# Kernel optimization log

Measured on AMD Instinct MI355X. Metric: run time of the kernel, lower is better.

The kernel has to match this reference:

```python
import jax, jax.numpy as jnp
import numpy as np

D_MODEL = 1024
NUM_HEADS = 16
D_K = D_MODEL // NUM_HEADS
B, S = 2, 2048


def setup_inputs() -> dict:
    key = jax.random.key(0)
    ks = jax.random.split(key, 9)
    scale = 1.0 / np.sqrt(D_MODEL)
    return {
        "hidden_states": jax.random.normal(ks[0], (B, S, D_MODEL), dtype=jnp.float32),
        "attention_mask": jnp.ones((B, S, S), dtype=jnp.int32),
        "Wq": jax.random.normal(ks[1], (D_MODEL, D_MODEL), dtype=jnp.float32) * scale,
        "bq": jnp.zeros((D_MODEL,), dtype=jnp.float32),
        "Wk": jax.random.normal(ks[2], (D_MODEL, D_MODEL), dtype=jnp.float32) * scale,
        "bk": jnp.zeros((D_MODEL,), dtype=jnp.float32),
        "Wv": jax.random.normal(ks[3], (D_MODEL, D_MODEL), dtype=jnp.float32) * scale,
        "bv": jnp.zeros((D_MODEL,), dtype=jnp.float32),
        "Wo": jax.random.normal(ks[4], (D_MODEL, D_MODEL), dtype=jnp.float32) * scale,
        "bo": jnp.zeros((D_MODEL,), dtype=jnp.float32),
    }


def reference(hidden_states, attention_mask, Wq, bq, Wk, bk, Wv, bv, Wo, bo):
    b, s, _ = hidden_states.shape
    # torch Linear: y = x @ W.T + b
    def proj(W, bias):
        y = jnp.einsum('bsd,ed->bse', hidden_states, W) + bias
        return y.reshape(b, s, NUM_HEADS, D_K).transpose(0, 2, 1, 3)  # [B,H,S,dk]
    q = proj(Wq, bq)
    k = proj(Wk, bk)
    v = proj(Wv, bv)
    scores = jnp.einsum('bnqd,bnkd->bnqk', q, k) / np.sqrt(D_K)
    mask = attention_mask[:, None, :, :]  # [B,1,S,S]
    scores = jnp.where(mask == 0, jnp.float32(-1e9), scores)
    attn = jax.nn.softmax(scores, axis=-1)  # dropout = identity (eval)
    ctx = jnp.einsum('bnqk,bnkd->bnqd', attn, v)
    ctx = ctx.transpose(0, 2, 1, 3).reshape(b, s, D_MODEL)
    return jnp.einsum('bsd,ed->bse', ctx, Wo) + bo
```

## Files before the change

### kernel.cpp

```cpp
#include <hip/hip_runtime.h>

typedef short short8 __attribute__((ext_vector_type(8)));
typedef float floatx4 __attribute__((ext_vector_type(4)));
typedef unsigned short ushort4v __attribute__((ext_vector_type(4)));

#define DEV static __device__ __forceinline__

DEV unsigned short f2bf(float f) {
  unsigned int u = __builtin_bit_cast(unsigned int, f);
  u += 0x7fffu + ((u >> 16) & 1u);
  return (unsigned short)(u >> 16);
}

DEV unsigned int pkbf2(float a, float b) {
  unsigned int ua = __builtin_bit_cast(unsigned int, a) + 0x8000u;
  unsigned int ub = __builtin_bit_cast(unsigned int, b) + 0x8000u;
  return (ua >> 16) | (ub & 0xffff0000u);
}

DEV void gload16(const unsigned short* g, unsigned short* l) {
  __builtin_amdgcn_global_load_lds((__attribute__((address_space(1))) void*)g,
                                   (__attribute__((address_space(3))) void*)l,
                                   16, 0, 0);
}

__global__ void convert_kernel(const float* __restrict__ hs, const float* __restrict__ Wq,
                               const float* __restrict__ Wk, const float* __restrict__ Wv,
                               const float* __restrict__ Wo,
                               unsigned short* __restrict__ xbf, unsigned short* __restrict__ wqkv,
                               unsigned short* __restrict__ wobf) {
  size_t i4 = ((size_t)blockIdx.x * 256 + threadIdx.x) * 4;
  const float* src;
  unsigned short* dst;
  if (i4 < 4194304) {
    src = hs + i4; dst = xbf + i4;
  } else if (i4 < 7340032) {
    size_t o = i4 - 4194304;
    size_t lo = o & 1048575;
    src = (o < 1048576) ? (Wq + lo) : ((o < 2097152) ? (Wk + lo) : (Wv + lo));
    dst = wqkv + o;
  } else {
    size_t o = i4 - 7340032;
    src = Wo + o; dst = wobf + o;
  }
  float4 v = *(const float4*)src;
  ushort4v u;
  u.x = f2bf(v.x); u.y = f2bf(v.y); u.z = f2bf(v.z); u.w = f2bf(v.w);
  *(ushort4v*)dst = u;
}

__global__ void maskpack_kernel(const int* __restrict__ mask, unsigned long long* __restrict__ bits) {
  int w = blockIdx.x * 256 + threadIdx.x;
  const int4* p = (const int4*)(mask + (size_t)w * 64);
  unsigned long long r = 0ull;
#pragma unroll
  for (int j = 0; j < 16; ++j) {
    int4 m = p[j];
    r |= (unsigned long long)(m.x != 0) << (j * 4 + 0);
    r |= (unsigned long long)(m.y != 0) << (j * 4 + 1);
    r |= (unsigned long long)(m.z != 0) << (j * 4 + 2);
    r |= (unsigned long long)(m.w != 0) << (j * 4 + 3);
  }
  bits[w] = r;
}

__global__ void __launch_bounds__(256) qkv_gemm(
    const unsigned short* __restrict__ X, const unsigned short* __restrict__ W,
    const float* __restrict__ bq, const float* __restrict__ bk, const float* __restrict__ bv,
    unsigned short* __restrict__ Qb, unsigned short* __restrict__ Kb,
    unsigned short* __restrict__ Vt) {
  __shared__ __align__(16) unsigned short As[128 * 32];
  __shared__ __align__(16) unsigned short Bs[128 * 32];
  const int tid = threadIdx.x;
  const int lane = tid & 63, wv = tid >> 6;
  const int wm = wv >> 1, wn = wv & 1;
  const int quad = lane >> 4, l15 = lane & 15;
  const int mb = blockIdx.y, nb = blockIdx.x;

  const unsigned short* ga = X + (size_t)(mb * 128 + (tid >> 2)) * 1024 + (tid & 3) * 8;
  const unsigned short* gb = W + (size_t)(nb * 128 + (tid >> 2)) * 1024 + (tid & 3) * 8;
  unsigned short* la1 = As + tid * 8;
  unsigned short* la2 = As + 2048 + tid * 8;
  unsigned short* lb1 = Bs + tid * 8;
  unsigned short* lb2 = Bs + 2048 + tid * 8;

  floatx4 acc[4][4] = {};
  for (int kt = 0; kt < 32; ++kt) {
    const int k0 = kt * 32;
    gload16(ga + k0, la1);
    gload16(ga + k0 + 65536, la2);
    gload16(gb + k0, lb1);
    gload16(gb + k0 + 65536, lb2);
    __syncthreads();
    short8 af[4], bfr[4];
#pragma unroll
    for (int i = 0; i < 4; ++i) {
      af[i]  = *(const short8*)&As[(wm * 64 + i * 16 + l15) * 32 + quad * 8];
      bfr[i] = *(const short8*)&Bs[(wn * 64 + i * 16 + l15) * 32 + quad * 8];
    }
#pragma unroll
    for (int mt = 0; mt < 4; ++mt)
#pragma unroll
      for (int nt = 0; nt < 4; ++nt)
        acc[mt][nt] = __builtin_amdgcn_mfma_f32_16x16x32_bf16(af[mt], bfr[nt], acc[mt][nt], 0, 0, 0);
    __syncthreads();
  }
#pragma unroll
  for (int nt = 0; nt < 4; ++nt) {
    const int col = nb * 128 + wn * 64 + nt * 16 + l15;
    const int mat = col >> 10, nl = col & 1023;
    const float bias = (mat == 0) ? bq[nl] : ((mat == 1) ? bk[nl] : bv[nl]);
    const int h = nl >> 6, d = nl & 63;
#pragma unroll
    for (int mt = 0; mt < 4; ++mt) {
      const int row0 = mb * 128 + wm * 64 + mt * 16 + quad * 4;
      const int b_ = row0 >> 11, s = row0 & 2047;
      if (mat == 2) {
        ushort4v pv;
#pragma unroll
        for (int r = 0; r < 4; ++r) pv[r] = f2bf(acc[mt][nt][r] + bias);
        *(ushort4v*)&Vt[((size_t)(b_ * 16 + h) * 64 + d) * 2048 + s] = pv;
      } else {
#pragma unroll
        for (int r = 0; r < 4; ++r) {
          const unsigned short v = f2bf(acc[mt][nt][r] + bias);
          if (mat == 0) Qb[((size_t)(b_ * 16 + h) * 2048 + s + r) * 64 + d] = v;
          else          Kb[((size_t)(b_ * 16 + h) * 2048 + s + r) * 64 + d] = v;
        }
      }
    }
  }
}

__global__ void __launch_bounds__(256, 4) attn_kernel(
    const unsigned short* __restrict__ Qb, const unsigned short* __restrict__ Kb,
    const unsigned short* __restrict__ Vt, const unsigned long long* __restrict__ mbits,
    unsigned short* __restrict__ ctx) {
  __shared__ __align__(16) unsigned short Ks[128 * 64];
  __shared__ __align__(16) unsigned short Vs[64 * 128];
  const int tid = threadIdx.x;
  const int lane = tid & 63, wv = tid >> 6;
  const int quad = lane >> 4, l15 = lane & 15;
  const int pair = blockIdx.x >> 5, qt = blockIdx.x & 31;
  const int b_ = pair >> 4, h = pair & 15;
  const int qg = qt * 64 + wv * 16 + l15;
  const size_t pbase = (size_t)pair * (2048 * 64);

  short8 qf[2];
#pragma unroll
  for (int ks = 0; ks < 2; ++ks)
    qf[ks] = *(const short8*)(Qb + pbase + (size_t)qg * 64 + ks * 32 + quad * 8);

  floatx4 acc_o[4] = {};
  float lsum = 0.f;
  const float SCL = 0.125f * 1.44269504088896340736f;
  const float NC = -10.0f;

  for (int kb = 0; kb < 16; ++kb) {
    __syncthreads();
#pragma unroll
    for (int it = 0; it < 4; ++it) {
      const int row = it * 32 + (tid >> 3);
      const int c = tid & 7;
      short8 v = *(const short8*)(Kb + pbase + (size_t)(kb * 128 + row) * 64 + c * 8);
      *(short8*)&Ks[row * 64 + ((c ^ (row & 7)) * 8)] = v;
    }
#pragma unroll
    for (int it = 0; it < 4; ++it) {
      const int row = it * 16 + (tid >> 4);
      const int c = tid & 15;
      short8 v = *(const short8*)(Vt + (size_t)pair * (64 * 2048) + (size_t)row * 2048 + kb * 128 + c * 8);
      *(short8*)&Vs[row * 128 + ((c ^ (row & 7)) * 8)] = v;
    }
    __syncthreads();

    const unsigned long long* mrow = mbits + ((size_t)b_ * 2048 + qg) * 32 + kb * 2;
    const unsigned long long w0 = mrow[0], w1 = mrow[1];

    floatx4 accs[8] = {};
#pragma unroll
    for (int ks = 0; ks < 2; ++ks)
#pragma unroll
      for (int mt = 0; mt < 8; ++mt) {
        const int krow = mt * 16 + l15;
        short8 kf = *(const short8*)&Ks[krow * 64 + (((ks * 4 + quad) ^ (krow & 7)) * 8)];
        accs[mt] = __builtin_amdgcn_mfma_f32_16x16x32_bf16(kf, qf[ks], accs[mt], 0, 0, 0);
      }

    if (__any((w0 & w1) != ~0ull)) {
      const unsigned long long wq0 = w0 >> (quad * 4);
      const unsigned long long wq1 = w1 >> (quad * 4);
#pragma unroll
      for (int ntb = 0; ntb < 8; ++ntb) {
        const unsigned long long w = (ntb < 4) ? wq0 : wq1;
#pragma unroll
        for (int r = 0; r < 4; ++r)
          if (!((w >> ((ntb & 3) * 16 + r)) & 1ull)) accs[ntb][r] = -6e9f;
      }
    }

    unsigned int pk[8][2];
#pragma unroll
    for (int ntb = 0; ntb < 8; ++ntb) {
      const float p0 = exp2f(fmaf(accs[ntb][0], SCL, NC));
      const float p1 = exp2f(fmaf(accs[ntb][1], SCL, NC));
      const float p2 = exp2f(fmaf(accs[ntb][2], SCL, NC));
      const float p3 = exp2f(fmaf(accs[ntb][3], SCL, NC));
      lsum += (p0 + p1) + (p2 + p3);
      pk[ntb][0] = pkbf2(p0, p1);
      pk[ntb][1] = pkbf2(p2, p3);
    }

#pragma unroll
    for (int ks = 0; ks < 4; ++ks) {
      const int srcA = (quad & 1) * 32 + l15;
      const int hi = quad >> 1;
      unsigned int u0a = __shfl(pk[2 * ks][0], srcA),      u0b = __shfl(pk[2 * ks + 1][0], srcA);
      unsigned int u1a = __shfl(pk[2 * ks][1], srcA),      u1b = __shfl(pk[2 * ks + 1][1], srcA);
      unsigned int u2a = __shfl(pk[2 * ks][0], srcA + 16), u2b = __shfl(pk[2 * ks + 1][0], srcA + 16);
      unsigned int u3a = __shfl(pk[2 * ks][1], srcA + 16), u3b = __shfl(pk[2 * ks + 1][1], srcA + 16);
      union { unsigned int u[4]; short8 s8; } af;
      af.u[0] = hi ? u0b : u0a;
      af.u[1] = hi ? u1b : u1a;
      af.u[2] = hi ? u2b : u2a;
      af.u[3] = hi ? u3b : u3a;
#pragma unroll
      for (int nt = 0; nt < 4; ++nt) {
        const int vrow = nt * 16 + l15;
        short8 vf = *(const short8*)&Vs[vrow * 128 + (((ks * 4 + quad) ^ (vrow & 7)) * 8)];
        acc_o[nt] = __builtin_amdgcn_mfma_f32_16x16x32_bf16(af.s8, vf, acc_o[nt], 0, 0, 0);
      }
    }
  }

  lsum += __shfl_xor(lsum, 16);
  lsum += __shfl_xor(lsum, 32);
  float rl[4];
#pragma unroll
  for (int r = 0; r < 4; ++r) {
    const float lr = __shfl(lsum, (lane & 48) | (quad * 4 + r));
    rl[r] = 1.f / ((lr > 0.f) ? lr : 1.f);
  }
#pragma unroll
  for (int nt = 0; nt < 4; ++nt)
#pragma unroll
    for (int r = 0; r < 4; ++r) {
      const int rowg = qt * 64 + wv * 16 + quad * 4 + r;
      ctx[((size_t)b_ * 2048 + rowg) * 1024 + h * 64 + nt * 16 + l15] =
          f2bf(acc_o[nt][r] * rl[r]);
    }
}

__global__ void __launch_bounds__(256) out_gemm(
    const unsigned short* __restrict__ C, const unsigned short* __restrict__ W,
    const float* __restrict__ bo, float* __restrict__ out) {
  __shared__ __align__(16) unsigned short As[128 * 32];
  __shared__ __align__(16) unsigned short Bs[128 * 32];
  const int tid = threadIdx.x;
  const int lane = tid & 63, wv = tid >> 6;
  const int wm = wv >> 1, wn = wv & 1;
  const int quad = lane >> 4, l15 = lane & 15;
  const int mb = blockIdx.y, nb = blockIdx.x;

  const unsigned short* ga = C + (size_t)(mb * 128 + (tid >> 2)) * 1024 + (tid & 3) * 8;
  const unsigned short* gb = W + (size_t)(nb * 128 + (tid >> 2)) * 1024 + (tid & 3) * 8;
  unsigned short* la1 = As + tid * 8;
  unsigned short* la2 = As + 2048 + tid * 8;
  unsigned short* lb1 = Bs + tid * 8;
  unsigned short* lb2 = Bs + 2048 + tid * 8;

  floatx4 acc[4][4] = {};
  for (int kt = 0; kt < 32; ++kt) {
    const int k0 = kt * 32;
    gload16(ga + k0, la1);
    gload16(ga + k0 + 65536, la2);
    gload16(gb + k0, lb1);
    gload16(gb + k0 + 65536, lb2);
    __syncthreads();
    short8 af[4], bfr[4];
#pragma unroll
    for (int i = 0; i < 4; ++i) {
      af[i]  = *(const short8*)&As[(wm * 64 + i * 16 + l15) * 32 + quad * 8];
      bfr[i] = *(const short8*)&Bs[(wn * 64 + i * 16 + l15) * 32 + quad * 8];
    }
#pragma unroll
    for (int mt = 0; mt < 4; ++mt)
#pragma unroll
      for (int nt = 0; nt < 4; ++nt)
        acc[mt][nt] = __builtin_amdgcn_mfma_f32_16x16x32_bf16(af[mt], bfr[nt], acc[mt][nt], 0, 0, 0);
    __syncthreads();
  }
#pragma unroll
  for (int nt = 0; nt < 4; ++nt) {
    const int col = nb * 128 + wn * 64 + nt * 16 + l15;
    const float bias = bo[col];
#pragma unroll
    for (int mt = 0; mt < 4; ++mt)
#pragma unroll
      for (int r = 0; r < 4; ++r) {
        const int row = mb * 128 + wm * 64 + mt * 16 + quad * 4 + r;
        out[(size_t)row * 1024 + col] = acc[mt][nt][r] + bias;
      }
  }
}

extern "C" void kernel_launch(void* const* d_in, const int* in_sizes, int n_in,
                              void* d_out, int out_size, void* d_ws, size_t ws_size,
                              hipStream_t stream) {
  const float* hs = (const float*)d_in[0];
  const int* mask = (const int*)d_in[1];
  const float* Wq = (const float*)d_in[2];
  const float* bq = (const float*)d_in[3];
  const float* Wk = (const float*)d_in[4];
  const float* bk = (const float*)d_in[5];
  const float* Wv = (const float*)d_in[6];
  const float* bv = (const float*)d_in[7];
  const float* Wo = (const float*)d_in[8];
  const float* bo = (const float*)d_in[9];
  float* out = (float*)d_out;

  char* ws = (char*)d_ws;
  unsigned short* xbf  = (unsigned short*)(ws + 0);
  unsigned short* wqkv = (unsigned short*)(ws + 8388608);
  unsigned short* wobf = (unsigned short*)(ws + 14680064);
  unsigned short* Qb   = (unsigned short*)(ws + 16777216);
  unsigned short* Kb   = (unsigned short*)(ws + 25165824);
  unsigned short* Vt   = (unsigned short*)(ws + 33554432);
  unsigned short* ctx  = (unsigned short*)(ws + 41943040);
  unsigned long long* mbits = (unsigned long long*)(ws + 50331648);

  convert_kernel<<<8192, 256, 0, stream>>>(hs, Wq, Wk, Wv, Wo, xbf, wqkv, wobf);
  maskpack_kernel<<<512, 256, 0, stream>>>(mask, mbits);
  qkv_gemm<<<dim3(24, 32), 256, 0, stream>>>(xbf, wqkv, bq, bk, bv, Qb, Kb, Vt);
  attn_kernel<<<1024, 256, 0, stream>>>(Qb, Kb, Vt, mbits, ctx);
  out_gemm<<<dim3(8, 32), 256, 0, stream>>>(ctx, wobf, bo, out);
}
```

Baseline: 269.6 us.

## Use 32x32 MFMA in attention with 2-wave blocks; vectorize Q/K stores in QKV GEMM

The attention kernel switches from 16x16x32 to 32x32x16 bf16 MFMA. Each of two waves now handles 32 query rows, and the P matrix is exchanged with a single xor-32 shuffle instead of many cross-lane shuffles. The V LDS swizzle is adjusted to match the new fragment layout. The QKV GEMM swaps operands for the Q/K column blocks so each lane writes four contiguous bf16 values as one vector store with float4 bias loads, instead of scattered 2-byte stores. The larger MFMA tiles raise register pressure, and smaller blocks change occupancy and per-block K/V load work.

```diff
diff --git a/kernel.cpp b/kernel.cpp
--- a/kernel.cpp
+++ b/kernel.cpp
@@ -2,6 +2,7 @@
 
 typedef short short8 __attribute__((ext_vector_type(8)));
 typedef float floatx4 __attribute__((ext_vector_type(4)));
+typedef float floatx16 __attribute__((ext_vector_type(16)));
 typedef unsigned short ushort4v __attribute__((ext_vector_type(4)));
 
 #define DEV static __device__ __forceinline__
@@ -76,6 +77,7 @@
   const int wm = wv >> 1, wn = wv & 1;
   const int quad = lane >> 4, l15 = lane & 15;
   const int mb = blockIdx.y, nb = blockIdx.x;
+  const bool sw = (nb < 16);
 
   const unsigned short* ga = X + (size_t)(mb * 128 + (tid >> 2)) * 1024 + (tid & 3) * 8;
   const unsigned short* gb = W + (size_t)(nb * 128 + (tid >> 2)) * 1024 + (tid & 3) * 8;
@@ -83,6 +85,9 @@
   unsigned short* la2 = As + 2048 + tid * 8;
   unsigned short* lb1 = Bs + tid * 8;
   unsigned short* lb2 = Bs + 2048 + tid * 8;
+
+  const int wx = sw ? wn : wm;
+  const int ww = sw ? wm : wn;
 
   floatx4 acc[4][4] = {};
   for (int kt = 0; kt < 32; ++kt) {
@@ -92,47 +97,70 @@
     gload16(gb + k0, lb1);
     gload16(gb + k0 + 65536, lb2);
     __syncthreads();
-    short8 af[4], bfr[4];
+    short8 xa[4], wb[4];
 #pragma unroll
     for (int i = 0; i < 4; ++i) {
-      af[i]  = *(const short8*)&As[(wm * 64 + i * 16 + l15) * 32 + quad * 8];
-      bfr[i] = *(const short8*)&Bs[(wn * 64 + i * 16 + l15) * 32 + quad * 8];
-    }
-#pragma unroll
-    for (int mt = 0; mt < 4; ++mt)
-#pragma unroll
-      for (int nt = 0; nt < 4; ++nt)
-        acc[mt][nt] = __builtin_amdgcn_mfma_f32_16x16x32_bf16(af[mt], bfr[nt], acc[mt][nt], 0, 0, 0);
-    __syncthreads();
-  }
-#pragma unroll
-  for (int nt = 0; nt < 4; ++nt) {
-    const int col = nb * 128 + wn * 64 + nt * 16 + l15;
-    const int mat = col >> 10, nl = col & 1023;
-    const float bias = (mat == 0) ? bq[nl] : ((mat == 1) ? bk[nl] : bv[nl]);
-    const int h = nl >> 6, d = nl & 63;
+      xa[i] = *(const short8*)&As[(wx * 64 + i * 16 + l15) * 32 + quad * 8];
+      wb[i] = *(const short8*)&Bs[(ww * 64 + i * 16 + l15) * 32 + quad * 8];
+    }
+    if (sw) {
+#pragma unroll
+      for (int mt = 0; mt < 4; ++mt)
+#pragma unroll
+        for (int nt = 0; nt < 4; ++nt)
+          acc[mt][nt] = __builtin_amdgcn_mfma_f32_16x16x32_bf16(wb[mt], xa[nt], acc[mt][nt], 0, 0, 0);
+    } else {
+#pragma unroll
+      for (int mt = 0; mt < 4; ++mt)
+#pragma unroll
+        for (int nt = 0; nt < 4; ++nt)
+          acc[mt][nt] = __builtin_amdgcn_mfma_f32_16x16x32_bf16(xa[mt], wb[nt], acc[mt][nt], 0, 0, 0);
+    }
+    __syncthreads();
+  }
+
+  if (sw) {
 #pragma unroll
     for (int mt = 0; mt < 4; ++mt) {
-      const int row0 = mb * 128 + wm * 64 + mt * 16 + quad * 4;
-      const int b_ = row0 >> 11, s = row0 & 2047;
-      if (mat == 2) {
+      const int wc0 = nb * 128 + wm * 64 + mt * 16 + quad * 4;
+      const int mat = wc0 >> 10;
+      const int nl0 = wc0 & 1023;
+      const int hh = nl0 >> 6, d0 = nl0 & 63;
+      const float4 b4 = *(const float4*)((mat ? bk : bq) + nl0);
+      unsigned short* dst = mat ? Kb : Qb;
+#pragma unroll
+      for (int nt = 0; nt < 4; ++nt) {
+        const int colx = mb * 128 + wn * 64 + nt * 16 + l15;
+        const int bb = colx >> 11, s = colx & 2047;
         ushort4v pv;
+        pv[0] = f2bf(acc[mt][nt][0] + b4.x);
+        pv[1] = f2bf(acc[mt][nt][1] + b4.y);
+        pv[2] = f2bf(acc[mt][nt][2] + b4.z);
+        pv[3] = f2bf(acc[mt][nt][3] + b4.w);
+        *(ushort4v*)&dst[((size_t)(bb * 16 + hh) * 2048 + s) * 64 + d0] = pv;
+      }
+    }
+  } else {
+#pragma unroll
+    for (int nt = 0; nt < 4; ++nt) {
+      const int col = nb * 128 + wn * 64 + nt * 16 + l15;
+      const int nl = col & 1023;
+      const float bias = bv[nl];
+      const int hh = nl >> 6, d = nl & 63;
+#pragma unroll
+      for (int mt = 0; mt < 4; ++mt) {
+        const int row0 = mb * 128 + wm * 64 + mt * 16 + quad * 4;
+        const int bb = row0 >> 11, s = row0 & 2047;
+        ushort4v pv;
 #pragma unroll
         for (int r = 0; r < 4; ++r) pv[r] = f2bf(acc[mt][nt][r] + bias);
-        *(ushort4v*)&Vt[((size_t)(b_ * 16 + h) * 64 + d) * 2048 + s] = pv;
-      } else {
-#pragma unroll
-        for (int r = 0; r < 4; ++r) {
-          const unsigned short v = f2bf(acc[mt][nt][r] + bias);
-          if (mat == 0) Qb[((size_t)(b_ * 16 + h) * 2048 + s + r) * 64 + d] = v;
-          else          Kb[((size_t)(b_ * 16 + h) * 2048 + s + r) * 64 + d] = v;
-        }
-      }
-    }
-  }
-}
-
-__global__ void __launch_bounds__(256, 4) attn_kernel(
+        *(ushort4v*)&Vt[((size_t)(bb * 16 + hh) * 64 + d) * 2048 + s] = pv;
+      }
+    }
+  }
+}
+
+__global__ void __launch_bounds__(128, 2) attn_kernel(
     const unsigned short* __restrict__ Qb, const unsigned short* __restrict__ Kb,
     const unsigned short* __restrict__ Vt, const unsigned long long* __restrict__ mbits,
     unsigned short* __restrict__ ctx) {
@@ -140,115 +168,111 @@
   __shared__ __align__(16) unsigned short Vs[64 * 128];
   const int tid = threadIdx.x;
   const int lane = tid & 63, wv = tid >> 6;
-  const int quad = lane >> 4, l15 = lane & 15;
+  const int l31 = lane & 31, h = lane >> 5;
   const int pair = blockIdx.x >> 5, qt = blockIdx.x & 31;
-  const int b_ = pair >> 4, h = pair & 15;
-  const int qg = qt * 64 + wv * 16 + l15;
+  const int b_ = pair >> 4, hd = pair & 15;
+  const int qg = qt * 64 + wv * 32 + l31;
   const size_t pbase = (size_t)pair * (2048 * 64);
 
-  short8 qf[2];
-#pragma unroll
-  for (int ks = 0; ks < 2; ++ks)
-    qf[ks] = *(const short8*)(Qb + pbase + (size_t)qg * 64 + ks * 32 + quad * 8);
-
-  floatx4 acc_o[4] = {};
+  short8 qf[4];
+#pragma unroll
+  for (int ks = 0; ks < 4; ++ks)
+    qf[ks] = *(const short8*)(Qb + pbase + (size_t)qg * 64 + ks * 16 + h * 8);
+
+  floatx16 acc_o[2] = {};
   float lsum = 0.f;
   const float SCL = 0.125f * 1.44269504088896340736f;
   const float NC = -10.0f;
 
-  for (int kb = 0; kb < 16; ++kb) {
-    __syncthreads();
-#pragma unroll
-    for (int it = 0; it < 4; ++it) {
-      const int row = it * 32 + (tid >> 3);
+  for (int kb16 = 0; kb16 < 16; ++kb16) {
+    __syncthreads();
+#pragma unroll
+    for (int it = 0; it < 8; ++it) {
+      const int row = it * 16 + (tid >> 3);
       const int c = tid & 7;
-      short8 v = *(const short8*)(Kb + pbase + (size_t)(kb * 128 + row) * 64 + c * 8);
+      short8 v = *(const short8*)(Kb + pbase + (size_t)(kb16 * 128 + row) * 64 + c * 8);
       *(short8*)&Ks[row * 64 + ((c ^ (row & 7)) * 8)] = v;
     }
 #pragma unroll
-    for (int it = 0; it < 4; ++it) {
-      const int row = it * 16 + (tid >> 4);
+    for (int it = 0; it < 8; ++it) {
+      const int row = it * 8 + (tid >> 4);
       const int c = tid & 15;
-      short8 v = *(const short8*)(Vt + (size_t)pair * (64 * 2048) + (size_t)row * 2048 + kb * 128 + c * 8);
-      *(short8*)&Vs[row * 128 + ((c ^ (row & 7)) * 8)] = v;
-    }
-    __syncthreads();
-
-    const unsigned long long* mrow = mbits + ((size_t)b_ * 2048 + qg) * 32 + kb * 2;
+      short8 v = *(const short8*)(Vt + (size_t)pair * (64 * 2048) + (size_t)row * 2048 + kb16 * 128 + c * 8);
+      *(short8*)&Vs[row * 128 + ((c ^ ((row & 7) << 1)) * 8)] = v;
+    }
+    __syncthreads();
+
+    const unsigned long long* mrow = mbits + ((size_t)b_ * 2048 + qg) * 32 + kb16 * 2;
     const unsigned long long w0 = mrow[0], w1 = mrow[1];
 
-    floatx4 accs[8] = {};
-#pragma unroll
-    for (int ks = 0; ks < 2; ++ks)
-#pragma unroll
-      for (int mt = 0; mt < 8; ++mt) {
-        const int krow = mt * 16 + l15;
-        short8 kf = *(const short8*)&Ks[krow * 64 + (((ks * 4 + quad) ^ (krow & 7)) * 8)];
-        accs[mt] = __builtin_amdgcn_mfma_f32_16x16x32_bf16(kf, qf[ks], accs[mt], 0, 0, 0);
+    floatx16 accs[4] = {};
+#pragma unroll
+    for (int ks = 0; ks < 4; ++ks)
+#pragma unroll
+      for (int kb = 0; kb < 4; ++kb) {
+        const int krow = kb * 32 + l31;
+        short8 kf = *(const short8*)&Ks[krow * 64 + (((ks * 2 + h) ^ (krow & 7)) * 8)];
+        accs[kb] = __builtin_amdgcn_mfma_f32_32x32x16_bf16(kf, qf[ks], accs[kb], 0, 0, 0);
       }
 
     if (__any((w0 & w1) != ~0ull)) {
-      const unsigned long long wq0 = w0 >> (quad * 4);
-      const unsigned long long wq1 = w1 >> (quad * 4);
-#pragma unroll
-      for (int ntb = 0; ntb < 8; ++ntb) {
-        const unsigned long long w = (ntb < 4) ? wq0 : wq1;
-#pragma unroll
-        for (int r = 0; r < 4; ++r)
-          if (!((w >> ((ntb & 3) * 16 + r)) & 1ull)) accs[ntb][r] = -6e9f;
-      }
-    }
-
-    unsigned int pk[8][2];
-#pragma unroll
-    for (int ntb = 0; ntb < 8; ++ntb) {
-      const float p0 = exp2f(fmaf(accs[ntb][0], SCL, NC));
-      const float p1 = exp2f(fmaf(accs[ntb][1], SCL, NC));
-      const float p2 = exp2f(fmaf(accs[ntb][2], SCL, NC));
-      const float p3 = exp2f(fmaf(accs[ntb][3], SCL, NC));
-      lsum += (p0 + p1) + (p2 + p3);
-      pk[ntb][0] = pkbf2(p0, p1);
-      pk[ntb][1] = pkbf2(p2, p3);
-    }
-
-#pragma unroll
-    for (int ks = 0; ks < 4; ++ks) {
-      const int srcA = (quad & 1) * 32 + l15;
-      const int hi = quad >> 1;
-      unsigned int u0a = __shfl(pk[2 * ks][0], srcA),      u0b = __shfl(pk[2 * ks + 1][0], srcA);
-      unsigned int u1a = __shfl(pk[2 * ks][1], srcA),      u1b = __shfl(pk[2 * ks + 1][1], srcA);
-      unsigned int u2a = __shfl(pk[2 * ks][0], srcA + 16), u2b = __shfl(pk[2 * ks + 1][0], srcA + 16);
-      unsigned int u3a = __shfl(pk[2 * ks][1], srcA + 16), u3b = __shfl(pk[2 * ks + 1][1], srcA + 16);
-      union { unsigned int u[4]; short8 s8; } af;
-      af.u[0] = hi ? u0b : u0a;
-      af.u[1] = hi ? u1b : u1a;
-      af.u[2] = hi ? u2b : u2a;
-      af.u[3] = hi ? u3b : u3a;
-#pragma unroll
-      for (int nt = 0; nt < 4; ++nt) {
-        const int vrow = nt * 16 + l15;
-        short8 vf = *(const short8*)&Vs[vrow * 128 + (((ks * 4 + quad) ^ (vrow & 7)) * 8)];
-        acc_o[nt] = __builtin_amdgcn_mfma_f32_16x16x32_bf16(af.s8, vf, acc_o[nt], 0, 0, 0);
-      }
-    }
-  }
-
-  lsum += __shfl_xor(lsum, 16);
+#pragma unroll
+      for (int kb = 0; kb < 4; ++kb) {
+        const unsigned long long w = (kb < 2) ? w0 : w1;
+#pragma unroll
+        for (int reg = 0; reg < 16; ++reg) {
+          const int kl = (reg & 3) + 8 * (reg >> 2) + 4 * h;
+          const int bit = (kb & 1) * 32 + kl;
+          if (!((w >> bit) & 1ull)) accs[kb][reg] = -6e9f;
+        }
+      }
+    }
+
+#pragma unroll
+    for (int kb = 0; kb < 4; ++kb) {
+      unsigned int pk[8];
+#pragma unroll
+      for (int i = 0; i < 8; ++i) {
+        const float a = exp2f(fmaf(accs[kb][2 * i], SCL, NC));
+        const float b = exp2f(fmaf(accs[kb][2 * i + 1], SCL, NC));
+        lsum += a + b;
+        pk[i] = pkbf2(a, b);
+      }
+#pragma unroll
+      for (int u = 0; u < 2; ++u) {
+        const unsigned int own0 = h ? pk[4 * u + 2] : pk[4 * u + 0];
+        const unsigned int own1 = h ? pk[4 * u + 3] : pk[4 * u + 1];
+        const unsigned int snd0 = h ? pk[4 * u + 0] : pk[4 * u + 2];
+        const unsigned int snd1 = h ? pk[4 * u + 1] : pk[4 * u + 3];
+        const unsigned int t0 = __shfl_xor(snd0, 32);
+        const unsigned int t1 = __shfl_xor(snd1, 32);
+        union { unsigned int w[4]; short8 s8; } af;
+        af.w[0] = h ? t0 : own0;
+        af.w[1] = h ? t1 : own1;
+        af.w[2] = h ? own0 : t0;
+        af.w[3] = h ? own1 : t1;
+        const int t = kb * 2 + u;
+#pragma unroll
+        for (int nt = 0; nt < 2; ++nt) {
+          const int vrow = nt * 32 + l31;
+          short8 vf = *(const short8*)&Vs[vrow * 128 + (((t * 2 + h) ^ ((vrow & 7) << 1)) * 8)];
+          acc_o[nt] = __builtin_amdgcn_mfma_f32_32x32x16_bf16(af.s8, vf, acc_o[nt], 0, 0, 0);
+        }
+      }
+    }
+  }
+
   lsum += __shfl_xor(lsum, 32);
-  float rl[4];
-#pragma unroll
-  for (int r = 0; r < 4; ++r) {
-    const float lr = __shfl(lsum, (lane & 48) | (quad * 4 + r));
-    rl[r] = 1.f / ((lr > 0.f) ? lr : 1.f);
-  }
-#pragma unroll
-  for (int nt = 0; nt < 4; ++nt)
-#pragma unroll
-    for (int r = 0; r < 4; ++r) {
-      const int rowg = qt * 64 + wv * 16 + quad * 4 + r;
-      ctx[((size_t)b_ * 2048 + rowg) * 1024 + h * 64 + nt * 16 + l15] =
-          f2bf(acc_o[nt][r] * rl[r]);
-    }
+  const float rinv = 1.f / ((lsum > 0.f) ? lsum : 1.f);
+
+#pragma unroll
+  for (int reg = 0; reg < 16; ++reg) {
+    const int ql = (reg & 3) + 8 * (reg >> 2) + 4 * h;
+    const float rl = __shfl(rinv, ql);
+    const size_t base = ((size_t)b_ * 2048 + qt * 64 + wv * 32 + ql) * 1024 + hd * 64;
+    ctx[base + l31]      = f2bf(acc_o[0][reg] * rl);
+    ctx[base + 32 + l31] = f2bf(acc_o[1][reg] * rl);
+  }
 }
 
 __global__ void __launch_bounds__(256) out_gemm(
@@ -332,6 +356,6 @@
   convert_kernel<<<8192, 256, 0, stream>>>(hs, Wq, Wk, Wv, Wo, xbf, wqkv, wobf);
   maskpack_kernel<<<512, 256, 0, stream>>>(mask, mbits);
   qkv_gemm<<<dim3(24, 32), 256, 0, stream>>>(xbf, wqkv, bq, bk, bv, Qb, Kb, Vt);
-  attn_kernel<<<1024, 256, 0, stream>>>(Qb, Kb, Vt, mbits, ctx);
+  attn_kernel<<<1024, 128, 0, stream>>>(Qb, Kb, Vt, mbits, ctx);
   out_gemm<<<dim3(8, 32), 256, 0, stream>>>(ctx, wobf, bo, out);
 }
```

Result: faster. 263.9 us (-2.1%).
